# Kernel optimization log

Hardware: AMD Instinct MI355X
Metric: run time of the kernel (lower is better)

The kernel has to match this reference:

```python
import jax, jax.numpy as jnp
import numpy as np

CONF_THRES = 0.25
IOU_THRES = 0.45
K = 1000          # fixed candidate count after confidence filter (pad/mask form of NMS)
MAX_WH = 4096.0   # class offset for class-aware (batched) NMS, as in yolov5


def _xywh2xyxy(b):
    cx, cy, w, h = b[..., 0], b[..., 1], b[..., 2], b[..., 3]
    return jnp.stack([cx - w * 0.5, cy - h * 0.5, cx + w * 0.5, cy + h * 0.5], axis=-1)


def _box_iou(a, b):
    # a: [K,4], b: [K,4] in xyxy -> [K,K] IoU
    area_a = (a[:, 2] - a[:, 0]) * (a[:, 3] - a[:, 1])
    area_b = (b[:, 2] - b[:, 0]) * (b[:, 3] - b[:, 1])
    lt = jnp.maximum(a[:, None, :2], b[None, :, :2])
    rb = jnp.minimum(a[:, None, 2:], b[None, :, 2:])
    wh = jnp.clip(rb - lt, 0.0)
    inter = wh[..., 0] * wh[..., 1]
    return inter / (area_a[:, None] + area_b[None, :] - inter + 1e-7)


def _nms_single(pred):
    # pred: [N, 5+C] = [cx,cy,w,h,obj, cls...]
    obj = pred[:, 4]
    cls_conf = obj[:, None] * pred[:, 5:]            # conf = obj * cls (yolov5)
    best = jnp.max(cls_conf, axis=-1)                # best-class score per box
    j = jnp.argmax(cls_conf, axis=-1)                # best class index
    valid = (obj > CONF_THRES) & (best > CONF_THRES)  # candidate + confidence filter
    score = jnp.where(valid, best, 0.0)

    vals, idx = jax.lax.top_k(score, K)              # descending -> greedy NMS order
    boxes = _xywh2xyxy(pred[:, :4])[idx]             # [K,4]
    cls = j[idx].astype(pred.dtype)                  # [K]

    off_boxes = boxes + (cls * MAX_WH)[:, None]      # class-aware offset
    iou = _box_iou(off_boxes, off_boxes)             # [K,K]

    ar = jnp.arange(K)

    def body(keep, inp):
        i, row = inp
        ki = keep[i]
        sup = (row > IOU_THRES) & (ar > i) & (ki > 0.5)
        return jnp.where(sup, 0.0, keep), None

    keep, _ = jax.lax.scan(body, jnp.ones((K,), pred.dtype), (ar, iou))

    final_score = vals * keep * (vals > CONF_THRES).astype(pred.dtype)
    # [K,6]: x1,y1,x2,y2,score,class ; suppressed/padded rows have score==0
    return jnp.concatenate([boxes, final_score[:, None], cls[:, None]], axis=-1)


def setup_inputs() -> dict:
    key = jax.random.key(0)
    B, N, C = 16, 25200, 85
    k1, k2 = jax.random.split(key)
    # plausible 640x640 detections: centers in [0,640), w/h in (0,100)
    xywh = jax.random.uniform(k1, (B, N, 4), dtype=jnp.float32) * jnp.array(
        [640.0, 640.0, 100.0, 100.0], dtype=jnp.float32)
    scores = jax.random.uniform(k2, (B, N, C - 4), dtype=jnp.float32)  # obj + 80 cls
    x = jnp.concatenate([xywh, scores], axis=-1)
    return {"x": x}


def reference(x):
    return jax.vmap(_nms_single)(x)  # [B, K, 6]
```

## Files before the change

### kernel.cpp

```cpp
#include <hip/hip_runtime.h>
#include <stdint.h>

#define BB 16
#define NN 25200
#define CC 85
#define NCLS 80
#define KK 1000
#define CAP 2048
#define NBIN 4096
#define BINBASE 0x3E800000u
#define TILE 84
#define NTILE 300
#define SBLK 384
#define CTILE 25
#define CNTSTRIDE 64
#define MBLK 40
#define RBLK 32
#define CONF 0.25f
#define IOUT 0.45f
#define MAXWH 4096.0f
#define NW 16
#define CHUNK 96

typedef unsigned long long u64;
typedef unsigned int u32;

__device__ __forceinline__ u64 umax64(u64 a, u64 b) { return a > b ? a : b; }

__device__ __forceinline__ u32 score_bin(u32 sb) {
  u32 d = (sb - BINBASE) >> 12;
  return d > (NBIN - 1) ? (NBIN - 1) : d;
}

__global__ __launch_bounds__(256) void k_zero(uint4* __restrict__ p, int n4) {
  int i = blockIdx.x * 256 + threadIdx.x;
  if (i < n4) p[i] = make_uint4(0u, 0u, 0u, 0u);
}

__global__ __launch_bounds__(SBLK) void k_score(const float* __restrict__ x,
                                                u64* __restrict__ keys,
                                                u32* __restrict__ hist) {
#pragma clang fp contract(off)
  __shared__ float tile[TILE * CC];
  __shared__ u32 zc;
  int b = blockIdx.x / NTILE;
  int t = blockIdx.x % NTILE;
  int tid = threadIdx.x;
  int base_row = t * TILE;
  const float4* src4 =
      (const float4*)(x + ((size_t)b * NN + base_row) * CC);
  float4* tile4 = (float4*)tile;
  if (tid == 0) zc = 0;
#pragma unroll
  for (int i = tid; i < TILE * CC / 4; i += SBLK) tile4[i] = src4[i];
  __syncthreads();

  if (tid < TILE * 4) {
    int row = tid >> 2, r = tid & 3;
    const float* rp = tile + row * CC;
    float obj = rp[4];
    float best = -1.0f;
    int bj = 0;
#pragma unroll
    for (int c = 0; c < 20; ++c) {
      float p = obj * rp[5 + r * 20 + c];
      if (p > best) { best = p; bj = r * 20 + c; }
    }
    u64 ck = ((u64)__float_as_uint(best) << 32) | (u32)(~(u32)bj);
    ck = umax64(ck, __shfl_xor(ck, 1));
    ck = umax64(ck, __shfl_xor(ck, 2));
    if (r == 0) {
      float bestv = __uint_as_float((u32)(ck >> 32));
      u32 j = ~(u32)(ck & 0xFFFFFFFFu);
      bool valid = (obj > CONF) && (bestv > CONF);
      float score = valid ? bestv : 0.0f;
      u32 sb = __float_as_uint(score);
      int n = base_row + row;
      u64 key = ((u64)sb << 32) | ((u64)(~(u32)n & 0xFFFFu) << 16) |
                ((u64)(j & 0xFFu) << 8);
      keys[(size_t)b * NN + n] = key;
      if (sb) {
        atomicAdd(&hist[b * NBIN + score_bin(sb)], 1u);
      } else {
        atomicAdd(&zc, 1u);
      }
    }
  }
  __syncthreads();
  if (tid == 0 && zc) atomicAdd(&hist[b * NBIN + 0], zc);
}

__global__ __launch_bounds__(1024) void k_pivot(const u32* __restrict__ hist,
                                                u32* __restrict__ pinfo) {
  __shared__ u32 s[1024];
  int b = blockIdx.x, tid = threadIdx.x;
  const uint4* h4 = (const uint4*)(hist + b * NBIN);
  uint4 v = h4[tid];
  u32 c = v.x + v.y + v.z + v.w;
  s[tid] = c;
  __syncthreads();
  u32 inc = c;
  for (int off = 1; off < 1024; off <<= 1) {
    u32 add = (tid + off < 1024) ? s[tid + off] : 0u;
    __syncthreads();
    inc += add;
    s[tid] = inc;
    __syncthreads();
  }
  if (inc >= KK && inc - c < KK) {
    u32 cum = inc - c;
    u32 hv[4] = {v.x, v.y, v.z, v.w};
    for (int i = 3; i >= 0; --i) {
      u32 hh = hv[i];
      if (cum + hh >= KK) { pinfo[b] = (u32)(tid * 4 + i); break; }
      cum += hh;
    }
  }
}

__global__ __launch_bounds__(1024) void k_compact2(const u64* __restrict__ keys,
                                                   const u32* __restrict__ pinfo,
                                                   u64* __restrict__ cand,
                                                   u32* __restrict__ cnt) {
  int b = blockIdx.x / CTILE;
  int t = blockIdx.x % CTILE;
  int tid = threadIdx.x;
  u32 pivot = pinfo[b];

  int n = t * 1024 + tid;
  bool cond = false;
  u64 key = 0;
  if (n < NN) {
    key = keys[(size_t)b * NN + n];
    u32 sb = (u32)(key >> 32);
    cond = sb && (score_bin(sb) >= pivot);
  }
  u64 m = __ballot(cond);
  if (!m) return;
  int lane = tid & 63;
  u32 prefix = (u32)__popcll(m & ((1ULL << lane) - 1ULL));
  u32 tot = (u32)__popcll(m);
  int leader = (int)__ffsll((long long)m) - 1;
  u32 base = 0;
  if (lane == leader) base = atomicAdd(&cnt[b * CNTSTRIDE], tot);
  base = (u32)__shfl((int)base, leader);
  if (cond) {
    u32 pos = base + prefix;
    if (pos < CAP) cand[(size_t)b * CAP + pos] = key;
  }
}

__global__ __launch_bounds__(256) void k_rank(const float* __restrict__ x,
                                              const u64* __restrict__ cand,
                                              const u32* __restrict__ cnt,
                                              float* __restrict__ out,
                                              float* __restrict__ offbox,
                                              float* __restrict__ vals) {
#pragma clang fp contract(off)
  __shared__ u64 lbuf[CAP];
  __shared__ u32 part[4][64];
  int b = blockIdx.x / RBLK;
  int chunk = blockIdx.x % RBLK;
  int tid = threadIdx.x;
  for (int i = tid; i < CAP; i += 256)
    lbuf[i] = cand[(size_t)b * CAP + i];
  __syncthreads();
  u32 total = cnt[b * CNTSTRIDE];
  if (total > CAP) total = CAP;

  int c = tid & 63;
  int seg = tid >> 6;
  int ci = chunk * 64 + c;
  u64 k = lbuf[ci];
  u32 pc = 0;
  if (k != 0ULL) {
    int j = seg;
#pragma unroll 4
    for (; j < (int)total; j += 4) pc += (lbuf[j] > k);
  }
  part[seg][c] = pc;
  __syncthreads();
  if (seg != 0) return;
  if (k == 0ULL) return;
  u32 rank = part[0][c] + part[1][c] + part[2][c] + part[3][c];
  if (rank >= KK) return;

  u32 ni = 65535u - (u32)((k >> 16) & 0xFFFFu);
  if (ni > NN - 1) ni = NN - 1;
  u32 cj = (u32)((k >> 8) & 0xFFu);
  float val = __uint_as_float((u32)(k >> 32));
  const float* row = x + ((size_t)b * NN + ni) * CC;
  float cx = row[0], cy = row[1], w = row[2], h = row[3];
  float x1 = cx - w * 0.5f, y1 = cy - h * 0.5f;
  float x2 = cx + w * 0.5f, y2 = cy + h * 0.5f;
  float cls = (float)cj;
  float off = cls * MAXWH;
  float* o = out + ((size_t)b * KK + rank) * 6;
  o[0] = x1; o[1] = y1; o[2] = x2; o[3] = y2; o[5] = cls;
  float* ob = offbox + ((size_t)b * KK + rank) * 4;
  ob[0] = x1 + off; ob[1] = y1 + off; ob[2] = x2 + off; ob[3] = y2 + off;
  vals[(size_t)b * KK + rank] = val;
}

__global__ __launch_bounds__(256) void k_mask(const float* __restrict__ offbox,
                                              u64* __restrict__ mask,
                                              u64* __restrict__ rowflag) {
#pragma clang fp contract(off)
  __shared__ float jx1[64], jy1[64], jx2[64], jy2[64], jar[64];
  int tid = threadIdx.x;
  int blk = blockIdx.x;
  int b = blk / MBLK;
  int s = blk % MBLK;
  int w = 0, r0 = 0;
  for (int g = 0; g < 16; ++g) {
    int nb = (g >> 2) + 1;
    if (s < nb) { w = g; r0 = s * 256; break; }
    s -= nb;
  }
  const float4* ob4 = (const float4*)(offbox + (size_t)b * KK * 4);
  if (tid < 64) {
    int j = w * 64 + tid;
    float4 v = (j < KK) ? ob4[j] : make_float4(0.f, 0.f, 0.f, 0.f);
    jx1[tid] = v.x; jy1[tid] = v.y; jx2[tid] = v.z; jy2[tid] = v.w;
    jar[tid] = (v.z - v.x) * (v.w - v.y);
  }
  __syncthreads();
  int i = r0 + tid;
  int rows_w = KK < 64 * (w + 1) ? KK : 64 * (w + 1);
  if (i >= rows_w) return;
  float4 A = ob4[i];
  float aa = (A.z - A.x) * (A.w - A.y);
  u64 bits = 0ULL;
  int j0 = w * 64;
#pragma unroll 4
  for (int jj = 0; jj < 64; ++jj) {
    int j = j0 + jj;
    if (j <= i) continue;
    float lx = fmaxf(A.x, jx1[jj]), ly = fmaxf(A.y, jy1[jj]);
    float rx = fminf(A.z, jx2[jj]), ry = fminf(A.w, jy2[jj]);
    float ww = rx - lx; ww = ww > 0.0f ? ww : 0.0f;
    float hh = ry - ly; hh = hh > 0.0f ? hh : 0.0f;
    float inter = ww * hh;
    float iou = inter / (aa + jar[jj] - inter + 1e-7f);
    if (iou > IOUT) bits |= (1ULL << jj);
  }
  mask[((size_t)b * KK + i) * NW + w] = bits;
  if (bits)
    atomicOr(&rowflag[(size_t)b * NW + (i >> 6)], 1ULL << (i & 63));
}

__global__ __launch_bounds__(64) void k_scan(const u64* __restrict__ mask,
                                             const u64* __restrict__ rowflag,
                                             const float* __restrict__ vals,
                                             float* __restrict__ out) {
  int b = blockIdx.x;
  int lane = threadIdx.x;
  int w = lane & 15;
  const u64* mb = mask + (size_t)b * KK * NW;
  __shared__ int rows[CHUNK];
  __shared__ u64 mrow[CHUNK][NW];
  __shared__ u64 skeep[NW];
  __shared__ int s_n;
  u64 keep = ~0ULL;

  u64 f0 = 0;
  int W0 = 0;
  if (lane == 0) f0 = rowflag[(size_t)b * NW + 0];

  while (true) {
    if (lane == 0) {
      int n = 0;
      while (n < CHUNK) {
        while (W0 < NW && f0 == 0ULL) {
          W0++;
          if (W0 < NW) f0 = rowflag[(size_t)b * NW + W0];
        }
        if (W0 >= NW) break;
        int bit = (int)__ffsll((long long)f0) - 1;
        f0 &= f0 - 1ULL;
        rows[n++] = W0 * 64 + bit;
      }
      s_n = n;
    }
    __syncthreads();
    int n = s_n;
    if (n > 0) {
      for (int r = lane >> 4; r < n; r += 4)
        mrow[r][lane & 15] = mb[(size_t)rows[r] * NW + (lane & 15)];
      __syncthreads();
      for (int idx = 0; idx < n; ++idx) {
        int i_ = rows[idx];
        int wi_ = i_ >> 6;
        u32 half_ = (i_ & 32) ? (u32)(keep >> 32) : (u32)keep;
        u32 kw_ = (u32)__builtin_amdgcn_readlane((int)half_, wi_);
        u32 bit_ = (kw_ >> (i_ & 31)) & 1u;
        keep &= bit_ ? ~mrow[idx][w] : ~0ULL;
      }
      __syncthreads();
    }
    if (n < CHUNK) break;
  }

  if (lane < NW) skeep[lane] = keep;
  __syncthreads();
  for (int s2 = lane; s2 < KK; s2 += 64) {
    float v = vals[(size_t)b * KK + s2];
    u64 kwv = skeep[s2 >> 6];
    float kbit = (float)((kwv >> (s2 & 63)) & 1ULL);
    float fs = v * kbit * (v > CONF ? 1.0f : 0.0f);
    out[((size_t)b * KK + s2) * 6 + 4] = fs;
  }
}

extern "C" void kernel_launch(void* const* d_in, const int* in_sizes, int n_in,
                              void* d_out, int out_size, void* d_ws,
                              size_t ws_size, hipStream_t stream) {
  const float* x = (const float*)d_in[0];
  float* out = (float*)d_out;
  char* ws = (char*)d_ws;
  (void)in_sizes; (void)n_in; (void)out_size; (void)ws_size;

  auto align256 = [](size_t v) { return (v + 255) & ~(size_t)255; };
  size_t keys_off = 0;
  size_t keys_sz = (size_t)BB * NN * 8;
  size_t hist_off = align256(keys_off + keys_sz);
  size_t hist_sz = (size_t)BB * NBIN * 4;
  size_t cand_off = hist_off + hist_sz;
  size_t cand_sz = (size_t)BB * CAP * 8;
  size_t cnt_off = cand_off + cand_sz;
  size_t cnt_sz = (size_t)BB * CNTSTRIDE * 4;
  size_t rowflag_off = cnt_off + cnt_sz;
  size_t rowflag_sz = (size_t)BB * NW * 8;
  size_t pinfo_off = rowflag_off + rowflag_sz;
  size_t pinfo_sz = 256;
  size_t mask_off = pinfo_off + pinfo_sz;
  size_t mask_sz = (size_t)BB * KK * NW * 8;
  size_t zero_sz = hist_sz + cand_sz + cnt_sz + rowflag_sz + pinfo_sz +
                   mask_sz;
  size_t offbox_off = align256(mask_off + mask_sz);
  size_t offbox_sz = (size_t)BB * KK * 4 * 4;
  size_t vals_off = align256(offbox_off + offbox_sz);

  u64* keys = (u64*)(ws + keys_off);
  u32* hist = (u32*)(ws + hist_off);
  u64* cand = (u64*)(ws + cand_off);
  u32* cnt = (u32*)(ws + cnt_off);
  u64* rowflag = (u64*)(ws + rowflag_off);
  u32* pinfo = (u32*)(ws + pinfo_off);
  u64* mask = (u64*)(ws + mask_off);
  float* offbox = (float*)(ws + offbox_off);
  float* vals = (float*)(ws + vals_off);

  int n4 = (int)(zero_sz / 16);
  k_zero<<<dim3((n4 + 255) / 256), dim3(256), 0, stream>>>(
      (uint4*)(ws + hist_off), n4);
  k_score<<<dim3(BB * NTILE), dim3(SBLK), 0, stream>>>(x, keys, hist);
  k_pivot<<<dim3(BB), dim3(1024), 0, stream>>>(hist, pinfo);
  k_compact2<<<dim3(BB * CTILE), dim3(1024), 0, stream>>>(keys, pinfo, cand,
                                                          cnt);
  k_rank<<<dim3(BB * RBLK), dim3(256), 0, stream>>>(x, cand, cnt, out, offbox,
                                                    vals);
  k_mask<<<dim3(BB * MBLK), dim3(256), 0, stream>>>(offbox, mask, rowflag);
  k_scan<<<dim3(BB), dim3(64), 0, stream>>>(mask, rowflag, vals, out);
}
```

Before: 82.89 us.

## Stage score tiles via direct global-to-LDS loads and stop zeroing mask buffer

```diff
diff --git a/kernel.cpp b/kernel.cpp
--- a/kernel.cpp
+++ b/kernel.cpp
@@ -22,6 +22,13 @@
 #define NW 16
 #define CHUNK 96
 
+#define STG_FULL 27648
+#define STG_TAIL4 57
+#define STG_FULL4 1728
+
+#define AS1(p) ((const __attribute__((address_space(1))) void*)(p))
+#define AS3(p) ((__attribute__((address_space(3))) void*)(p))
+
 typedef unsigned long long u64;
 typedef unsigned int u32;
 
@@ -47,12 +54,17 @@
   int t = blockIdx.x % NTILE;
   int tid = threadIdx.x;
   int base_row = t * TILE;
-  const float4* src4 =
-      (const float4*)(x + ((size_t)b * NN + base_row) * CC);
+  const char* gb = (const char*)(x + ((size_t)b * NN + base_row) * CC);
+  const float4* src4 = (const float4*)gb;
   float4* tile4 = (float4*)tile;
   if (tid == 0) zc = 0;
-#pragma unroll
-  for (int i = tid; i < TILE * CC / 4; i += SBLK) tile4[i] = src4[i];
+
+  int wv = tid >> 6, ln = tid & 63;
+  for (int off = wv * 1024; off < STG_FULL; off += 6 * 1024) {
+    __builtin_amdgcn_global_load_lds(AS1(gb + off + ln * 16),
+                                     AS3((char*)tile + off), 16, 0, 0);
+  }
+  if (tid < STG_TAIL4) tile4[STG_FULL4 + tid] = src4[STG_FULL4 + tid];
   __syncthreads();
 
   if (tid < TILE * 4) {
@@ -241,8 +253,8 @@
     float ww = rx - lx; ww = ww > 0.0f ? ww : 0.0f;
     float hh = ry - ly; hh = hh > 0.0f ? hh : 0.0f;
     float inter = ww * hh;
-    float iou = inter / (aa + jar[jj] - inter + 1e-7f);
-    if (iou > IOUT) bits |= (1ULL << jj);
+    float denom = aa + jar[jj] - inter + 1e-7f;
+    if (inter > IOUT * denom) bits |= (1ULL << jj);
   }
   mask[((size_t)b * KK + i) * NW + w] = bits;
   if (bits)
@@ -285,8 +297,11 @@
     __syncthreads();
     int n = s_n;
     if (n > 0) {
-      for (int r = lane >> 4; r < n; r += 4)
-        mrow[r][lane & 15] = mb[(size_t)rows[r] * NW + (lane & 15)];
+      for (int r = lane >> 4; r < n; r += 4) {
+        int word = lane & 15;
+        u64 v = mb[(size_t)rows[r] * NW + word];
+        mrow[r][word] = (word < (rows[r] >> 6)) ? 0ULL : v;
+      }
       __syncthreads();
       for (int idx = 0; idx < n; ++idx) {
         int i_ = rows[idx];
@@ -333,13 +348,14 @@
   size_t rowflag_sz = (size_t)BB * NW * 8;
   size_t pinfo_off = rowflag_off + rowflag_sz;
   size_t pinfo_sz = 256;
-  size_t mask_off = pinfo_off + pinfo_sz;
-  size_t mask_sz = (size_t)BB * KK * NW * 8;
-  size_t zero_sz = hist_sz + cand_sz + cnt_sz + rowflag_sz + pinfo_sz +
-                   mask_sz;
-  size_t offbox_off = align256(mask_off + mask_sz);
+  size_t zero_sz = hist_sz + cand_sz + cnt_sz + rowflag_sz + pinfo_sz;
+  size_t offbox_off = align256(pinfo_off + pinfo_sz);
   size_t offbox_sz = (size_t)BB * KK * 4 * 4;
   size_t vals_off = align256(offbox_off + offbox_sz);
+  size_t vals_sz = (size_t)BB * KK * 4;
+  size_t mask_off = align256(vals_off + vals_sz);
+  size_t mask_sz = (size_t)BB * KK * NW * 8;
+  (void)mask_sz;
 
   u64* keys = (u64*)(ws + keys_off);
   u32* hist = (u32*)(ws + hist_off);
@@ -347,9 +363,9 @@
   u32* cnt = (u32*)(ws + cnt_off);
   u64* rowflag = (u64*)(ws + rowflag_off);
   u32* pinfo = (u32*)(ws + pinfo_off);
-  u64* mask = (u64*)(ws + mask_off);
   float* offbox = (float*)(ws + offbox_off);
   float* vals = (float*)(ws + vals_off);
+  u64* mask = (u64*)(ws + mask_off);
 
   int n4 = (int)(zero_sz / 16);
   k_zero<<<dim3((n4 + 255) / 256), dim3(256), 0, stream>>>(
```

New measurement: 75.71 us. -8.7%, faster.
